# Performance work log

Hardware: AMD Instinct MI355X
Metric: run time of the kernel (lower is better)

## Reference

```python
import jax, jax.numpy as jnp
import numpy as np

B, S, D, H = 4, 1024, 1024, 16
HD = D // H  # head_dim = 64
MASKED_BIAS = -10000.0


def setup_inputs() -> dict:
    key = jax.random.key(0)
    ks = jax.random.split(key, 7)
    sc = 0.02
    return {
        "hidden_states": jax.random.normal(ks[0], (B, S, D), jnp.float32),
        "textual_key": jax.random.normal(ks[1], (B, H, S, HD), jnp.float32),
        "textual_value": jax.random.normal(ks[2], (B, H, S, HD), jnp.float32),
        "Wc": jax.random.normal(ks[3], (D, 3 * D), jnp.float32) * sc,  # Conv1D c_attn
        "bc": jnp.zeros((3 * D,), jnp.float32),
        "Wp": jax.random.normal(ks[4], (D, D), jnp.float32) * sc,  # Conv1D c_proj
        "bp": jnp.zeros((D,), jnp.float32),
    }


def reference(hidden_states, textual_key, textual_value, Wc, bc, Wp, bp):
    b, s, d = hidden_states.shape
    # Conv1D: x @ W + b, then split into q, k, v
    qkv = hidden_states @ Wc + bc  # [B,S,3D]
    q, k, v = jnp.split(qkv, 3, axis=-1)

    def split_heads(t):  # [B,S,D] -> [B,H,S,HD]
        return t.reshape(b, s, H, HD).transpose(0, 2, 1, 3)

    q, k, v = split_heads(q), split_heads(k), split_heads(v)

    # cross-key scores against textual past + fused elementwise self-term
    text_w = jnp.einsum("bhqd,bhkd->bhqk", q, textual_key)  # [B,H,S,S_kv]
    self_w = jnp.sum(q * k, axis=-1, keepdims=True)  # [B,H,S,1]
    attn_w = jnp.concatenate([text_w, self_w], axis=-1) / (HD ** 0.5)

    # nonResidual causal mask: bias[kl-ql:kl, 1:kl+1] (strict lower-tri since
    # columns are shifted by 1) concatenated with an always-true self column
    i = jnp.arange(s)
    causal = i[None, :] < i[:, None]  # [S,S_kv]: allow k < q (strict)
    mask = jnp.concatenate([causal, jnp.ones((s, 1), bool)], axis=-1)[None, None]
    attn_w = jnp.where(mask, attn_w, jnp.asarray(MASKED_BIAS, attn_w.dtype))
    attn_w = jax.nn.softmax(attn_w, axis=-1)

    w_rest, w_self = attn_w[..., :-1], attn_w[..., -1:]
    out = jnp.einsum("bhqk,bhkd->bhqd", w_rest, textual_value) + w_self * v

    out = out.transpose(0, 2, 1, 3).reshape(b, s, d)  # merge heads
    return out @ Wp + bp
```

## Files before the change

### kernel.cpp

```cpp
#include <hip/hip_runtime.h>

typedef __bf16 bf16_t;
typedef __bf16 bf16x8 __attribute__((ext_vector_type(8)));
typedef __bf16 bf16x4 __attribute__((ext_vector_type(4)));
typedef _Float16 f16x4 __attribute__((ext_vector_type(4)));
typedef float f32x4 __attribute__((ext_vector_type(4)));

__device__ __forceinline__ void gl_lds16(const void* g, void* l) {
  __builtin_amdgcn_global_load_lds(
      (const __attribute__((address_space(1))) unsigned int*)g,
      (__attribute__((address_space(3))) unsigned int*)l, 16, 0, 0);
}

__global__ __launch_bounds__(256) void prep_kernel(
    const float* __restrict__ hs, const float* __restrict__ tk, const float* __restrict__ tv,
    const float* __restrict__ Wc, const float* __restrict__ Wp,
    bf16_t* __restrict__ Ahs, bf16_t* __restrict__ Ktb, _Float16* __restrict__ Vtb,
    bf16_t* __restrict__ WcT, bf16_t* __restrict__ WpT) {
  const int blk = blockIdx.x;
  if (blk < 8192) {
    const float4* src = (blk < 4096) ? (const float4*)hs : (const float4*)tk;
    bf16x4* dst = (blk < 4096) ? (bf16x4*)Ahs : (bf16x4*)Ktb;
    int i = (blk & 4095) * 256 + threadIdx.x;
    float4 v = src[i];
    bf16x4 o;
    o[0] = (bf16_t)v.x; o[1] = (bf16_t)v.y; o[2] = (bf16_t)v.z; o[3] = (bf16_t)v.w;
    dst[i] = o;
  } else {
    __shared__ float tile[32][33];
    const int x = threadIdx.x & 31, y0 = threadIdx.x >> 5;
    const float* in; bf16_t* out; int C, c0, r0; size_t base; bool isV = false;
    if (blk < 11264) {
      int t = blk - 8192; in = Wc; out = WcT; C = 3072; base = 0;
      c0 = (t % 96) * 32; r0 = (t / 96) * 32;
    } else if (blk < 12288) {
      int t = blk - 11264; in = Wp; out = WpT; C = 1024; base = 0;
      c0 = (t & 31) * 32; r0 = (t >> 5) * 32;
    } else {
      int t = blk - 12288; int z = t >> 6, rest = t & 63;
      in = tv; out = nullptr; isV = true; C = 64; base = (size_t)z * 65536;
      c0 = (rest & 1) * 32; r0 = (rest >> 1) * 32;
    }
#pragma unroll
    for (int k = 0; k < 4; k++) {
      int y = y0 + 8 * k;
      tile[y][x] = in[base + (size_t)(r0 + y) * C + c0 + x];
    }
    __syncthreads();
#pragma unroll
    for (int k = 0; k < 4; k++) {
      int y = y0 + 8 * k;
      if (isV)
        Vtb[base + (size_t)(c0 + y) * 1024 + r0 + x] = (_Float16)tile[x][y];
      else
        out[base + (size_t)(c0 + y) * 1024 + r0 + x] = (bf16_t)tile[x][y];
    }
  }
}

__global__ __launch_bounds__(256) void gemm_qkv_kernel(
    const bf16_t* __restrict__ A, const bf16_t* __restrict__ Bt, const float* __restrict__ bias,
    bf16_t* __restrict__ Qo, bf16_t* __restrict__ Ko, bf16_t* __restrict__ Vo) {
  __shared__ __align__(16) bf16_t Asm[128 * 64];
  __shared__ __align__(16) bf16_t Bsm[128 * 64];
  const int tid = threadIdx.x;
  const int wave = tid >> 6, lane = tid & 63;
  const int c = lane & 15, qd = lane >> 4;
  const int wm = (wave & 1) * 64, wn = (wave >> 1) * 64;
  const int id = blockIdx.y * 24 + blockIdx.x;
  const int xcd = id & 7, idx = id >> 3;
  const int n0 = (xcd * 3 + (idx % 3)) * 128, m0 = (idx / 3) * 128;

  f32x4 acc[4][4];
#pragma unroll
  for (int i = 0; i < 4; i++)
#pragma unroll
    for (int j = 0; j < 4; j++) acc[i][j] = (f32x4){0.f, 0.f, 0.f, 0.f};

  for (int kt = 0; kt < 1024; kt += 64) {
#pragma unroll
    for (int p = 0; p < 4; p++) {
      int chunk = p * 256 + tid;
      int row = chunk >> 3, sb = chunk & 7;
      int kb = sb ^ (row & 7);
      gl_lds16(A + (size_t)(m0 + row) * 1024 + kt + kb * 8, &Asm[chunk * 8]);
      gl_lds16(Bt + (size_t)(n0 + row) * 1024 + kt + kb * 8, &Bsm[chunk * 8]);
    }
    __syncthreads();
#pragma unroll
    for (int kk = 0; kk < 2; kk++) {
      bf16x8 af[4], bfr[4];
#pragma unroll
      for (int i = 0; i < 4; i++) {
        int row = wm + 16 * i + c;
        af[i] = *(const bf16x8*)(&Asm[row * 64 + (((4 * kk + qd) ^ (row & 7)) << 3)]);
      }
#pragma unroll
      for (int j = 0; j < 4; j++) {
        int row = wn + 16 * j + c;
        bfr[j] = *(const bf16x8*)(&Bsm[row * 64 + (((4 * kk + qd) ^ (row & 7)) << 3)]);
      }
#pragma unroll
      for (int i = 0; i < 4; i++)
#pragma unroll
        for (int j = 0; j < 4; j++)
          acc[i][j] = __builtin_amdgcn_mfma_f32_16x16x32_bf16(af[i], bfr[j], acc[i][j], 0, 0, 0);
    }
    __syncthreads();
  }
#pragma unroll
  for (int j = 0; j < 4; j++) {
    int n = n0 + wn + 16 * j + c;
    float bv = bias[n];
    int type = n >> 10, d = n & 1023;
    int h = d >> 6, hd = d & 63;
    bf16_t* dst = (type == 0) ? Qo : (type == 1) ? Ko : Vo;
#pragma unroll
    for (int i = 0; i < 4; i++) {
#pragma unroll
      for (int r = 0; r < 4; r++) {
        int m = m0 + wm + 16 * i + 4 * qd + r;
        int bb = m >> 10, s = m & 1023;
        dst[(((size_t)bb * 16 + h) * 1024 + s) * 64 + hd] = (bf16_t)(acc[i][j][r] + bv);
      }
    }
  }
}

__global__ __launch_bounds__(256) void gemm_out_kernel(
    const bf16_t* __restrict__ A, const bf16_t* __restrict__ Bt, const float* __restrict__ bias,
    float* __restrict__ out) {
  __shared__ bf16_t Asm[2][4096];
  __shared__ bf16_t Bsm[2][8192];
  const int tid = threadIdx.x;
  const int wave = tid >> 6, lane = tid & 63;
  const int c = lane & 15, qd = lane >> 4;
  const int wn = wave * 32;
  const int m0 = blockIdx.y * 64, n0 = blockIdx.x * 128;

  f32x4 acc[4][2];
#pragma unroll
  for (int i = 0; i < 4; i++)
#pragma unroll
    for (int j = 0; j < 2; j++) acc[i][j] = (f32x4){0.f, 0.f, 0.f, 0.f};

#pragma unroll
  for (int p = 0; p < 2; p++) {
    int chunk = p * 256 + tid;
    int row = chunk >> 3, sb = chunk & 7, kb = sb ^ (row & 7);
    gl_lds16(A + (size_t)(m0 + row) * 1024 + kb * 8, &Asm[0][chunk * 8]);
  }
#pragma unroll
  for (int p = 0; p < 4; p++) {
    int chunk = p * 256 + tid;
    int row = chunk >> 3, sb = chunk & 7, kb = sb ^ (row & 7);
    gl_lds16(Bt + (size_t)(n0 + row) * 1024 + kb * 8, &Bsm[0][chunk * 8]);
  }
  for (int it = 0; it < 16; it++) {
    __syncthreads();
    if (it < 15) {
      int nbuf = (it + 1) & 1, kt = (it + 1) * 64;
#pragma unroll
      for (int p = 0; p < 2; p++) {
        int chunk = p * 256 + tid;
        int row = chunk >> 3, sb = chunk & 7, kb = sb ^ (row & 7);
        gl_lds16(A + (size_t)(m0 + row) * 1024 + kt + kb * 8, &Asm[nbuf][chunk * 8]);
      }
#pragma unroll
      for (int p = 0; p < 4; p++) {
        int chunk = p * 256 + tid;
        int row = chunk >> 3, sb = chunk & 7, kb = sb ^ (row & 7);
        gl_lds16(Bt + (size_t)(n0 + row) * 1024 + kt + kb * 8, &Bsm[nbuf][chunk * 8]);
      }
    }
    const int bs = it & 1;
#pragma unroll
    for (int kk = 0; kk < 2; kk++) {
      bf16x8 af[4], bfr[2];
#pragma unroll
      for (int i = 0; i < 4; i++) {
        int row = 16 * i + c;
        af[i] = *(const bf16x8*)(&Asm[bs][row * 64 + (((4 * kk + qd) ^ (row & 7)) << 3)]);
      }
#pragma unroll
      for (int j = 0; j < 2; j++) {
        int row = wn + 16 * j + c;
        bfr[j] = *(const bf16x8*)(&Bsm[bs][row * 64 + (((4 * kk + qd) ^ (row & 7)) << 3)]);
      }
#pragma unroll
      for (int i = 0; i < 4; i++)
#pragma unroll
        for (int j = 0; j < 2; j++)
          acc[i][j] = __builtin_amdgcn_mfma_f32_16x16x32_bf16(af[i], bfr[j], acc[i][j], 0, 0, 0);
    }
  }
#pragma unroll
  for (int j = 0; j < 2; j++) {
    int n = n0 + wn + 16 * j + c;
    float bv = bias[n];
#pragma unroll
    for (int i = 0; i < 4; i++) {
#pragma unroll
      for (int r = 0; r < 4; r++) {
        int m = m0 + 16 * i + 4 * qd + r;
        out[(size_t)m * 1024 + n] = acc[i][j][r] + bv;
      }
    }
  }
}

#define ATTN_M 12.0f
__global__ __launch_bounds__(512) void attn_kernel(
    const bf16_t* __restrict__ Q, const bf16_t* __restrict__ K, const bf16_t* __restrict__ V,
    const bf16_t* __restrict__ Ktxt, const _Float16* __restrict__ VtxtT,
    bf16_t* __restrict__ Aout) {
  const int bh = blockIdx.x;
  const int qt = blockIdx.y;
  const int b = bh >> 4, h = bh & 15;
  const int tid = threadIdx.x, wave = tid >> 6, lane = tid & 63;
  const int c = lane & 15, qd = lane >> 4;
  const int i_base = qt * 128 + wave * 16;
  const int kt_max = 2 * qt + 1;

  const bf16_t* Qb = Q + (size_t)bh * 65536;
  const bf16_t* Kb = K + (size_t)bh * 65536;
  const bf16_t* Vb = V + (size_t)bh * 65536;
  const bf16_t* Ktb = Ktxt + (size_t)bh * 65536;
  const _Float16* Vtb = VtxtT + (size_t)bh * 65536;

  __shared__ bf16_t Ksm[2][4096];
  __shared__ _Float16 Vsm[2][4096];

  {
    int row = tid >> 3, sb = tid & 7, kb = sb ^ (row & 7);
    gl_lds16(Ktb + (size_t)row * 64 + kb * 8, &Ksm[0][tid * 8]);
    gl_lds16(Vtb + (size_t)row * 1024 + kb * 8, &Vsm[0][tid * 8]);
  }

  bf16x8 aq[2], kf0, kf1;
  {
    const size_t ro = (size_t)(i_base + c) * 64;
    aq[0] = *(const bf16x8*)(Qb + ro + 8 * qd);
    aq[1] = *(const bf16x8*)(Qb + ro + 32 + 8 * qd);
    kf0 = *(const bf16x8*)(Kb + ro + 8 * qd);
    kf1 = *(const bf16x8*)(Kb + ro + 32 + 8 * qd);
  }
  float part = 0.f;
#pragma unroll
  for (int jj = 0; jj < 8; jj++)
    part += (float)aq[0][jj] * (float)kf0[jj] + (float)aq[1][jj] * (float)kf1[jj];
  part += __shfl_xor(part, 16, 64);
  part += __shfl_xor(part, 32, 64);

  float wself[4];
  float l_loc = 0.f;
  f32x4 O[4];
#pragma unroll
  for (int r = 0; r < 4; r++)
    wself[r] = __expf(__shfl(part, 4 * qd + r, 64) * 0.125f - ATTN_M);
#pragma unroll
  for (int u = 0; u < 4; u++)
#pragma unroll
    for (int r = 0; r < 4; r++)
      O[u][r] = wself[r] * (float)Vb[(size_t)(i_base + 4 * qd + r) * 64 + 16 * u + c];

  for (int kt = 0; kt <= kt_max; kt++) {
    __syncthreads();
    if (kt < kt_max) {
      int nb = (kt + 1) & 1;
      int row = tid >> 3, sb = tid & 7, kb = sb ^ (row & 7);
      gl_lds16(Ktb + (size_t)((kt + 1) * 64 + row) * 64 + kb * 8, &Ksm[nb][tid * 8]);
      gl_lds16(Vtb + (size_t)row * 1024 + (kt + 1) * 64 + kb * 8, &Vsm[nb][tid * 8]);
    }
    if (64 * kt >= i_base + 16) continue;
    const int bs = kt & 1;

    f32x4 sc[4];
#pragma unroll
    for (int t = 0; t < 4; t++) sc[t] = (f32x4){0.f, 0.f, 0.f, 0.f};
#pragma unroll
    for (int kk = 0; kk < 2; kk++) {
#pragma unroll
      for (int t = 0; t < 4; t++) {
        int row = 16 * t + c;
        bf16x8 bk = *(const bf16x8*)(&Ksm[bs][row * 64 + (((4 * kk + qd) ^ (row & 7)) << 3)]);
        sc[t] = __builtin_amdgcn_mfma_f32_16x16x32_bf16(bk, aq[kk], sc[t], 0, 0, 0);
      }
    }
    const bool edge = (64 * kt + 63 >= i_base);
    f16x4 pa[4];
    if (!edge) {
#pragma unroll
      for (int t = 0; t < 4; t++)
#pragma unroll
        for (int r = 0; r < 4; r++) {
          float p = __expf(sc[t][r] * 0.125f - ATTN_M);
          l_loc += p;
          pa[t][r] = (_Float16)p;
        }
    } else {
#pragma unroll
      for (int t = 0; t < 4; t++)
#pragma unroll
        for (int r = 0; r < 4; r++) {
          bool masked = (64 * kt + 16 * t + 4 * qd + r >= i_base + c);
          float p = masked ? 0.f : __expf(sc[t][r] * 0.125f - ATTN_M);
          l_loc += p;
          pa[t][r] = (_Float16)p;
        }
    }
#pragma unroll
    for (int u = 0; u < 4; u++) {
      int row = 16 * u + c;
#pragma unroll
      for (int t = 0; t < 4; t++) {
        int kc = 2 * t + (qd >> 1);
        f16x4 vb = *(const f16x4*)(&Vsm[bs][row * 64 + ((kc ^ (row & 7)) << 3) + ((qd & 1) << 2)]);
        O[u] = __builtin_amdgcn_mfma_f32_16x16x16f16(pa[t], vb, O[u], 0, 0, 0);
      }
    }
  }

  l_loc += __shfl_xor(l_loc, 16, 64);
  l_loc += __shfl_xor(l_loc, 32, 64);
#pragma unroll
  for (int r = 0; r < 4; r++) {
    float lq = __shfl(l_loc, 4 * qd + r, 16);
    float inv = 1.0f / (lq + wself[r]);
    int i = i_base + 4 * qd + r;
#pragma unroll
    for (int u = 0; u < 4; u++)
      Aout[((size_t)b * 1024 + i) * 1024 + h * 64 + 16 * u + c] = (bf16_t)(O[u][r] * inv);
  }
}

extern "C" void kernel_launch(void* const* d_in, const int* in_sizes, int n_in,
                              void* d_out, int out_size, void* d_ws, size_t ws_size,
                              hipStream_t stream) {
  const float* hs = (const float*)d_in[0];
  const float* tk = (const float*)d_in[1];
  const float* tv = (const float*)d_in[2];
  const float* Wc = (const float*)d_in[3];
  const float* bc = (const float*)d_in[4];
  const float* Wp = (const float*)d_in[5];
  const float* bp = (const float*)d_in[6];
  float* out = (float*)d_out;

  bf16_t* ws = (bf16_t*)d_ws;
  const size_t M1 = 1u << 20;
  bf16_t* Ahs  = ws;
  bf16_t* WcT  = ws + 4 * M1;
  bf16_t* WpT  = ws + 7 * M1;
  bf16_t* Ktb  = ws + 8 * M1;
  _Float16* Vtb = (_Float16*)(ws + 12 * M1);
  bf16_t* Qb   = ws + 16 * M1;
  bf16_t* Kb   = ws + 20 * M1;
  bf16_t* Vb   = ws + 24 * M1;
  bf16_t* Aout = ws + 28 * M1;

  prep_kernel<<<16384, 256, 0, stream>>>(hs, tk, tv, Wc, Wp, Ahs, Ktb, Vtb, WcT, WpT);
  gemm_qkv_kernel<<<dim3(24, 32), 256, 0, stream>>>(Ahs, WcT, bc, Qb, Kb, Vb);
  attn_kernel<<<dim3(64, 8), 512, 0, stream>>>(Qb, Kb, Vb, Ktb, Vtb, Aout);
  gemm_out_kernel<<<dim3(8, 64), 256, 0, stream>>>(Aout, WpT, bp, out);
}
```

Before: 200.1 us.

## Fuse QKV projection GEMM into attention kernel per head tile

Each attention block now computes its 128x192 slice of the QKV projection directly from bf16 hidden states and weights, keeping Q, K and V in registers and LDS instead of writing them to global memory. The self-term dot product and V initialisation come from the accumulators, and Q is staged through LDS to get MFMA operand layout. This removes a kernel launch and the global round-trip of Q/K/V, but the in-block GEMM uses a narrow 16-row-per-wave tiling with single-buffered loads, which may be less efficient than the standalone GEMM.

```diff
diff --git a/kernel.cpp b/kernel.cpp
--- a/kernel.cpp
+++ b/kernel.cpp
@@ -58,72 +58,179 @@
   }
 }
 
-__global__ __launch_bounds__(256) void gemm_qkv_kernel(
-    const bf16_t* __restrict__ A, const bf16_t* __restrict__ Bt, const float* __restrict__ bias,
-    bf16_t* __restrict__ Qo, bf16_t* __restrict__ Ko, bf16_t* __restrict__ Vo) {
-  __shared__ __align__(16) bf16_t Asm[128 * 64];
-  __shared__ __align__(16) bf16_t Bsm[128 * 64];
-  const int tid = threadIdx.x;
-  const int wave = tid >> 6, lane = tid & 63;
+#define ATTN_M 12.0f
+__global__ __launch_bounds__(512, 4) void fused_attn_kernel(
+    const bf16_t* __restrict__ Ahs, const bf16_t* __restrict__ WcT,
+    const float* __restrict__ bc,
+    const bf16_t* __restrict__ Ktxt, const _Float16* __restrict__ VtxtT,
+    bf16_t* __restrict__ Aout) {
+  const int bh = blockIdx.x;
+  const int qt = blockIdx.y;
+  const int b = bh >> 4, h = bh & 15;
+  const int tid = threadIdx.x, wave = tid >> 6, lane = tid & 63;
   const int c = lane & 15, qd = lane >> 4;
-  const int wm = (wave & 1) * 64, wn = (wave >> 1) * 64;
-  const int id = blockIdx.y * 24 + blockIdx.x;
-  const int xcd = id & 7, idx = id >> 3;
-  const int n0 = (xcd * 3 + (idx % 3)) * 128, m0 = (idx / 3) * 128;
-
-  f32x4 acc[4][4];
-#pragma unroll
-  for (int i = 0; i < 4; i++)
-#pragma unroll
-    for (int j = 0; j < 4; j++) acc[i][j] = (f32x4){0.f, 0.f, 0.f, 0.f};
-
-  for (int kt = 0; kt < 1024; kt += 64) {
-#pragma unroll
-    for (int p = 0; p < 4; p++) {
-      int chunk = p * 256 + tid;
-      int row = chunk >> 3, sb = chunk & 7;
-      int kb = sb ^ (row & 7);
-      gl_lds16(A + (size_t)(m0 + row) * 1024 + kt + kb * 8, &Asm[chunk * 8]);
-      gl_lds16(Bt + (size_t)(n0 + row) * 1024 + kt + kb * 8, &Bsm[chunk * 8]);
+  const int i_base = qt * 128 + wave * 16;
+  const int kt_max = 2 * qt + 1;
+  const int m0 = b * 1024 + qt * 128;
+
+  const bf16_t* Ktb = Ktxt + (size_t)bh * 65536;
+  const _Float16* Vtb = VtxtT + (size_t)bh * 65536;
+
+  __shared__ __align__(16) char pool[49152];
+  bf16_t* Asm = (bf16_t*)pool;
+  bf16_t* Bsm = (bf16_t*)(pool + 16384);
+  bf16_t* Qsm = (bf16_t*)pool;
+  bf16_t* KsmB = (bf16_t*)(pool + 16384);
+  _Float16* VsmB = (_Float16*)(pool + 32768);
+
+  f32x4 acc[12];
+#pragma unroll
+  for (int j = 0; j < 12; j++) acc[j] = (f32x4){0.f, 0.f, 0.f, 0.f};
+
+  for (int kt = 0; kt < 16; kt++) {
+#pragma unroll
+    for (int p = 0; p < 2; p++) {
+      int chunk = p * 512 + tid;
+      int row = chunk >> 3, sb = chunk & 7, kb = sb ^ (row & 7);
+      gl_lds16(Ahs + (size_t)(m0 + row) * 1024 + kt * 64 + kb * 8, Asm + chunk * 8);
+    }
+#pragma unroll
+    for (int p = 0; p < 3; p++) {
+      int chunk = p * 512 + tid;
+      int brow = chunk >> 3, sb = chunk & 7, kb = sb ^ (brow & 7);
+      int wrow = (brow >> 6) * 1024 + h * 64 + (brow & 63);
+      gl_lds16(WcT + (size_t)wrow * 1024 + kt * 64 + kb * 8, Bsm + chunk * 8);
     }
     __syncthreads();
 #pragma unroll
     for (int kk = 0; kk < 2; kk++) {
-      bf16x8 af[4], bfr[4];
-#pragma unroll
-      for (int i = 0; i < 4; i++) {
-        int row = wm + 16 * i + c;
-        af[i] = *(const bf16x8*)(&Asm[row * 64 + (((4 * kk + qd) ^ (row & 7)) << 3)]);
-      }
-#pragma unroll
-      for (int j = 0; j < 4; j++) {
-        int row = wn + 16 * j + c;
-        bfr[j] = *(const bf16x8*)(&Bsm[row * 64 + (((4 * kk + qd) ^ (row & 7)) << 3)]);
-      }
-#pragma unroll
-      for (int i = 0; i < 4; i++)
-#pragma unroll
-        for (int j = 0; j < 4; j++)
-          acc[i][j] = __builtin_amdgcn_mfma_f32_16x16x32_bf16(af[i], bfr[j], acc[i][j], 0, 0, 0);
-    }
-    __syncthreads();
-  }
+      int arow = wave * 16 + c;
+      bf16x8 af = *(const bf16x8*)(&Asm[arow * 64 + (((4 * kk + qd) ^ (arow & 7)) << 3)]);
+#pragma unroll
+      for (int j = 0; j < 12; j++) {
+        int brow = 16 * j + c;
+        bf16x8 bf = *(const bf16x8*)(&Bsm[brow * 64 + (((4 * kk + qd) ^ (brow & 7)) << 3)]);
+        acc[j] = __builtin_amdgcn_mfma_f32_16x16x32_bf16(af, bf, acc[j], 0, 0, 0);
+      }
+    }
+    __syncthreads();
+  }
+
+  {
+    int row = tid >> 3, sb = tid & 7, kb = sb ^ (row & 7);
+    gl_lds16(Ktb + (size_t)row * 64 + kb * 8, KsmB + tid * 8);
+    gl_lds16(Vtb + (size_t)row * 1024 + kb * 8, VsmB + tid * 8);
+  }
+
+#pragma unroll
+  for (int j = 0; j < 12; j++) {
+    float bv = bc[(j >> 2) * 1024 + h * 64 + 16 * (j & 3) + c];
+#pragma unroll
+    for (int r = 0; r < 4; r++) acc[j][r] += bv;
+  }
+
+  float wself[4];
+#pragma unroll
+  for (int r = 0; r < 4; r++) {
+    float part = acc[0][r] * acc[4][r] + acc[1][r] * acc[5][r] +
+                 acc[2][r] * acc[6][r] + acc[3][r] * acc[7][r];
+#pragma unroll
+    for (int mk = 1; mk < 16; mk <<= 1) part += __shfl_xor(part, mk, 64);
+    wself[r] = __expf(part * 0.125f - ATTN_M);
+  }
+
+  f32x4 O[4];
+#pragma unroll
+  for (int u = 0; u < 4; u++)
+#pragma unroll
+    for (int r = 0; r < 4; r++) O[u][r] = wself[r] * acc[8 + u][r];
+
+  bf16_t* Qw = Qsm + wave * 1024;
 #pragma unroll
   for (int j = 0; j < 4; j++) {
-    int n = n0 + wn + 16 * j + c;
-    float bv = bias[n];
-    int type = n >> 10, d = n & 1023;
-    int h = d >> 6, hd = d & 63;
-    bf16_t* dst = (type == 0) ? Qo : (type == 1) ? Ko : Vo;
-#pragma unroll
-    for (int i = 0; i < 4; i++) {
-#pragma unroll
-      for (int r = 0; r < 4; r++) {
-        int m = m0 + wm + 16 * i + 4 * qd + r;
-        int bb = m >> 10, s = m & 1023;
-        dst[(((size_t)bb * 16 + h) * 1024 + s) * 64 + hd] = (bf16_t)(acc[i][j][r] + bv);
-      }
-    }
+#pragma unroll
+    for (int r = 0; r < 4; r++) {
+      int ql = 4 * qd + r, d = 16 * j + c;
+      int ch = (d >> 3) ^ (ql & 7);
+      Qw[ql * 64 + (ch << 3) + (d & 7)] = (bf16_t)acc[j][r];
+    }
+  }
+  bf16x8 aq[2];
+#pragma unroll
+  for (int kk = 0; kk < 2; kk++) {
+    int ch = (4 * kk + qd) ^ (c & 7);
+    aq[kk] = *(const bf16x8*)(&Qw[c * 64 + (ch << 3)]);
+  }
+
+  float l_loc = 0.f;
+  for (int kt = 0; kt <= kt_max; kt++) {
+    __syncthreads();
+    if (kt < kt_max) {
+      int nb = (kt + 1) & 1;
+      int row = tid >> 3, sb = tid & 7, kb = sb ^ (row & 7);
+      gl_lds16(Ktb + (size_t)((kt + 1) * 64 + row) * 64 + kb * 8, KsmB + nb * 4096 + tid * 8);
+      gl_lds16(Vtb + (size_t)row * 1024 + (kt + 1) * 64 + kb * 8, VsmB + nb * 4096 + tid * 8);
+    }
+    if (64 * kt >= i_base + 16) continue;
+    const bf16_t* Ks = KsmB + (kt & 1) * 4096;
+    const _Float16* Vs = VsmB + (kt & 1) * 4096;
+
+    f32x4 sc[4];
+#pragma unroll
+    for (int t = 0; t < 4; t++) sc[t] = (f32x4){0.f, 0.f, 0.f, 0.f};
+#pragma unroll
+    for (int kk = 0; kk < 2; kk++) {
+#pragma unroll
+      for (int t = 0; t < 4; t++) {
+        int row = 16 * t + c;
+        bf16x8 bk = *(const bf16x8*)(&Ks[row * 64 + (((4 * kk + qd) ^ (row & 7)) << 3)]);
+        sc[t] = __builtin_amdgcn_mfma_f32_16x16x32_bf16(bk, aq[kk], sc[t], 0, 0, 0);
+      }
+    }
+    const bool edge = (64 * kt + 63 >= i_base);
+    f16x4 pa[4];
+    if (!edge) {
+#pragma unroll
+      for (int t = 0; t < 4; t++)
+#pragma unroll
+        for (int r = 0; r < 4; r++) {
+          float p = __expf(sc[t][r] * 0.125f - ATTN_M);
+          l_loc += p;
+          pa[t][r] = (_Float16)p;
+        }
+    } else {
+#pragma unroll
+      for (int t = 0; t < 4; t++)
+#pragma unroll
+        for (int r = 0; r < 4; r++) {
+          bool masked = (64 * kt + 16 * t + 4 * qd + r >= i_base + c);
+          float p = masked ? 0.f : __expf(sc[t][r] * 0.125f - ATTN_M);
+          l_loc += p;
+          pa[t][r] = (_Float16)p;
+        }
+    }
+#pragma unroll
+    for (int u = 0; u < 4; u++) {
+      int row = 16 * u + c;
+#pragma unroll
+      for (int t = 0; t < 4; t++) {
+        int kc = 2 * t + (qd >> 1);
+        f16x4 vb = *(const f16x4*)(&Vs[row * 64 + ((kc ^ (row & 7)) << 3) + ((qd & 1) << 2)]);
+        O[u] = __builtin_amdgcn_mfma_f32_16x16x16f16(pa[t], vb, O[u], 0, 0, 0);
+      }
+    }
+  }
+
+  l_loc += __shfl_xor(l_loc, 16, 64);
+  l_loc += __shfl_xor(l_loc, 32, 64);
+#pragma unroll
+  for (int r = 0; r < 4; r++) {
+    float lq = __shfl(l_loc, 4 * qd + r, 16);
+    float inv = 1.0f / (lq + wself[r]);
+    int i = i_base + 4 * qd + r;
+#pragma unroll
+    for (int u = 0; u < 4; u++)
+      Aout[((size_t)b * 1024 + i) * 1024 + h * 64 + 16 * u + c] = (bf16_t)(O[u][r] * inv);
   }
 }
 
@@ -206,131 +313,6 @@
         out[(size_t)m * 1024 + n] = acc[i][j][r] + bv;
       }
     }
-  }
-}
-
-#define ATTN_M 12.0f
-__global__ __launch_bounds__(512) void attn_kernel(
-    const bf16_t* __restrict__ Q, const bf16_t* __restrict__ K, const bf16_t* __restrict__ V,
-    const bf16_t* __restrict__ Ktxt, const _Float16* __restrict__ VtxtT,
-    bf16_t* __restrict__ Aout) {
-  const int bh = blockIdx.x;
-  const int qt = blockIdx.y;
-  const int b = bh >> 4, h = bh & 15;
-  const int tid = threadIdx.x, wave = tid >> 6, lane = tid & 63;
-  const int c = lane & 15, qd = lane >> 4;
-  const int i_base = qt * 128 + wave * 16;
-  const int kt_max = 2 * qt + 1;
-
-  const bf16_t* Qb = Q + (size_t)bh * 65536;
-  const bf16_t* Kb = K + (size_t)bh * 65536;
-  const bf16_t* Vb = V + (size_t)bh * 65536;
-  const bf16_t* Ktb = Ktxt + (size_t)bh * 65536;
-  const _Float16* Vtb = VtxtT + (size_t)bh * 65536;
-
-  __shared__ bf16_t Ksm[2][4096];
-  __shared__ _Float16 Vsm[2][4096];
-
-  {
-    int row = tid >> 3, sb = tid & 7, kb = sb ^ (row & 7);
-    gl_lds16(Ktb + (size_t)row * 64 + kb * 8, &Ksm[0][tid * 8]);
-    gl_lds16(Vtb + (size_t)row * 1024 + kb * 8, &Vsm[0][tid * 8]);
-  }
-
-  bf16x8 aq[2], kf0, kf1;
-  {
-    const size_t ro = (size_t)(i_base + c) * 64;
-    aq[0] = *(const bf16x8*)(Qb + ro + 8 * qd);
-    aq[1] = *(const bf16x8*)(Qb + ro + 32 + 8 * qd);
-    kf0 = *(const bf16x8*)(Kb + ro + 8 * qd);
-    kf1 = *(const bf16x8*)(Kb + ro + 32 + 8 * qd);
-  }
-  float part = 0.f;
-#pragma unroll
-  for (int jj = 0; jj < 8; jj++)
-    part += (float)aq[0][jj] * (float)kf0[jj] + (float)aq[1][jj] * (float)kf1[jj];
-  part += __shfl_xor(part, 16, 64);
-  part += __shfl_xor(part, 32, 64);
-
-  float wself[4];
-  float l_loc = 0.f;
-  f32x4 O[4];
-#pragma unroll
-  for (int r = 0; r < 4; r++)
-    wself[r] = __expf(__shfl(part, 4 * qd + r, 64) * 0.125f - ATTN_M);
-#pragma unroll
-  for (int u = 0; u < 4; u++)
-#pragma unroll
-    for (int r = 0; r < 4; r++)
-      O[u][r] = wself[r] * (float)Vb[(size_t)(i_base + 4 * qd + r) * 64 + 16 * u + c];
-
-  for (int kt = 0; kt <= kt_max; kt++) {
-    __syncthreads();
-    if (kt < kt_max) {
-      int nb = (kt + 1) & 1;
-      int row = tid >> 3, sb = tid & 7, kb = sb ^ (row & 7);
-      gl_lds16(Ktb + (size_t)((kt + 1) * 64 + row) * 64 + kb * 8, &Ksm[nb][tid * 8]);
-      gl_lds16(Vtb + (size_t)row * 1024 + (kt + 1) * 64 + kb * 8, &Vsm[nb][tid * 8]);
-    }
-    if (64 * kt >= i_base + 16) continue;
-    const int bs = kt & 1;
-
-    f32x4 sc[4];
-#pragma unroll
-    for (int t = 0; t < 4; t++) sc[t] = (f32x4){0.f, 0.f, 0.f, 0.f};
-#pragma unroll
-    for (int kk = 0; kk < 2; kk++) {
-#pragma unroll
-      for (int t = 0; t < 4; t++) {
-        int row = 16 * t + c;
-        bf16x8 bk = *(const bf16x8*)(&Ksm[bs][row * 64 + (((4 * kk + qd) ^ (row & 7)) << 3)]);
-        sc[t] = __builtin_amdgcn_mfma_f32_16x16x32_bf16(bk, aq[kk], sc[t], 0, 0, 0);
-      }
-    }
-    const bool edge = (64 * kt + 63 >= i_base);
-    f16x4 pa[4];
-    if (!edge) {
-#pragma unroll
-      for (int t = 0; t < 4; t++)
-#pragma unroll
-        for (int r = 0; r < 4; r++) {
-          float p = __expf(sc[t][r] * 0.125f - ATTN_M);
-          l_loc += p;
-          pa[t][r] = (_Float16)p;
-        }
-    } else {
-#pragma unroll
-      for (int t = 0; t < 4; t++)
-#pragma unroll
-        for (int r = 0; r < 4; r++) {
-          bool masked = (64 * kt + 16 * t + 4 * qd + r >= i_base + c);
-          float p = masked ? 0.f : __expf(sc[t][r] * 0.125f - ATTN_M);
-          l_loc += p;
-          pa[t][r] = (_Float16)p;
-        }
-    }
-#pragma unroll
-    for (int u = 0; u < 4; u++) {
-      int row = 16 * u + c;
-#pragma unroll
-      for (int t = 0; t < 4; t++) {
-        int kc = 2 * t + (qd >> 1);
-        f16x4 vb = *(const f16x4*)(&Vsm[bs][row * 64 + ((kc ^ (row & 7)) << 3) + ((qd & 1) << 2)]);
-        O[u] = __builtin_amdgcn_mfma_f32_16x16x16f16(pa[t], vb, O[u], 0, 0, 0);
-      }
-    }
-  }
-
-  l_loc += __shfl_xor(l_loc, 16, 64);
-  l_loc += __shfl_xor(l_loc, 32, 64);
-#pragma unroll
-  for (int r = 0; r < 4; r++) {
-    float lq = __shfl(l_loc, 4 * qd + r, 16);
-    float inv = 1.0f / (lq + wself[r]);
-    int i = i_base + 4 * qd + r;
-#pragma unroll
-    for (int u = 0; u < 4; u++)
-      Aout[((size_t)b * 1024 + i) * 1024 + h * 64 + 16 * u + c] = (bf16_t)(O[u][r] * inv);
   }
 }
 
@@ -353,13 +335,9 @@
   bf16_t* WpT  = ws + 7 * M1;
   bf16_t* Ktb  = ws + 8 * M1;
   _Float16* Vtb = (_Float16*)(ws + 12 * M1);
-  bf16_t* Qb   = ws + 16 * M1;
-  bf16_t* Kb   = ws + 20 * M1;
-  bf16_t* Vb   = ws + 24 * M1;
   bf16_t* Aout = ws + 28 * M1;
 
   prep_kernel<<<16384, 256, 0, stream>>>(hs, tk, tv, Wc, Wp, Ahs, Ktb, Vtb, WcT, WpT);
-  gemm_qkv_kernel<<<dim3(24, 32), 256, 0, stream>>>(Ahs, WcT, bc, Qb, Kb, Vb);
-  attn_kernel<<<dim3(64, 8), 512, 0, stream>>>(Qb, Kb, Vb, Ktb, Vtb, Aout);
+  fused_attn_kernel<<<dim3(64, 8), 512, 0, stream>>>(Ahs, WcT, bc, Ktb, Vtb, Aout);
   gemm_out_kernel<<<dim3(8, 64), 256, 0, stream>>>(Aout, WpT, bp, out);
 }
```

Measured after the change: 177.3 us. 11.4% less time.
